# Optimization experiments

Hardware: AMD Instinct MI355X
Metric: run time of the kernel (lower is better)

The kernel has to match this reference:

```python
import jax, jax.numpy as jnp
import numpy as np

B, C, H, W = 4, 512, 32, 32
HEADS = 8
EPS = 1e-5


def setup_inputs() -> dict:
    key = jax.random.key(0)
    ks = jax.random.split(key, 9)
    s = 1.0 / np.sqrt(C)
    return {
        "x": jax.random.normal(ks[0], (B, C, H, W), dtype=jnp.float32),
        "w_q": jax.random.normal(ks[1], (C, C), dtype=jnp.float32) * s,  # Conv2d 1x1, no bias
        "w_k": jax.random.normal(ks[2], (C, C), dtype=jnp.float32) * s,
        "w_v": jax.random.normal(ks[3], (C, C), dtype=jnp.float32) * s,
        "w_head": jax.random.normal(ks[4], (HEADS, HEADS), dtype=jnp.float32) * (1.0 / np.sqrt(HEADS)),
        "in_gamma": jnp.ones((HEADS,), dtype=jnp.float32) + 0.1 * jax.random.normal(ks[5], (HEADS,), dtype=jnp.float32),
        "in_beta": 0.1 * jax.random.normal(ks[6], (HEADS,), dtype=jnp.float32),
        "w_proj": jax.random.normal(ks[7], (C, C), dtype=jnp.float32) * s,
        "b_proj": 0.02 * jax.random.normal(ks[8], (C,), dtype=jnp.float32),
    }


def reference(x, w_q, w_k, w_v, w_head, in_gamma, in_beta, w_proj, b_proj):
    b, c, h, w = x.shape
    heads = w_head.shape[0]
    hd = c // heads
    t = h * w
    scale = hd ** (-0.5)

    xf = x.reshape(b, c, t)  # [B,C,T]
    # 1x1 convs == channel matmuls
    q = jnp.einsum('oc,bct->bot', w_q, xf).reshape(b, heads, hd, t)
    k = jnp.einsum('oc,bct->bot', w_k, xf).reshape(b, heads, hd, t)
    v = jnp.einsum('oc,bct->bot', w_v, xf).reshape(b, heads, hd, t)

    attn = jnp.einsum('bhdq,bhdT->bhqT', q, k) * scale           # [B,heads,T,T]
    attn = jnp.einsum('gh,bhqT->bgqT', w_head, attn)             # head-mixing 1x1 conv
    attn = jax.nn.softmax(attn, axis=-1)
    # InstanceNorm2d over the (T,T) spatial dims, per head, biased variance
    mean = jnp.mean(attn, axis=(-2, -1), keepdims=True)
    var = jnp.var(attn, axis=(-2, -1), keepdims=True)
    attn = (attn - mean) / jnp.sqrt(var + EPS)
    attn = attn * in_gamma[None, :, None, None] + in_beta[None, :, None, None]

    out = jnp.einsum('bhqT,bhdT->bhqd', attn, v)                 # [B,heads,T,hd]
    out = out.reshape(b, t, c)                                   # same row-major flatten as torch .view
    out = out @ w_proj.T + b_proj                                # Linear
    return out.transpose(0, 2, 1).reshape(b, c, h, w)
```

## Files before the change

kernel.cpp:

```cpp
#include <hip/hip_runtime.h>
#include <hip/hip_bf16.h>

#define B_ 4
#define C_ 512
#define T_ 1024
#define SCALE_ 0.125f
#define EPS_ 1e-5f

typedef unsigned short u16;
typedef __attribute__((ext_vector_type(8))) unsigned short u16x8;
typedef __attribute__((ext_vector_type(4))) unsigned short u16x4;
typedef __attribute__((ext_vector_type(8))) short s16x8;
typedef __attribute__((ext_vector_type(4))) float f32x4;

#define QT_OFF    (0x0ull)
#define KS_OFF    (0x400000ull)
#define VS_OFF    (0x800000ull)
#define XT_OFF    (0xC00000ull)
#define O_OFF     (0x1000000ull)
#define AB_OFF    (0x1410000ull)
#define VSUM_OFF  (0x1420000ull)
#define BIAS2_OFF (0x1430000ull)
#define LSUM_OFF  (0x1440000ull)
#define L2SUM_OFF (0x1460000ull)
#define WB_OFF    (0x1480000ull)
#define LP_OFF    (0x1680000ull)
#define L2P_OFF   (0x1700000ull)
#define WS_OFF    (0x1780000ull)
#define OP_OFF    (0x2000000ull)

static __device__ __forceinline__ u16 f2bf(float f) {
  unsigned u = __float_as_uint(f);
  unsigned r = (u + 0x7fff + ((u >> 16) & 1)) >> 16;
  return (u16)r;
}
static __device__ __forceinline__ float b2f(u16 x) {
  return __uint_as_float(((unsigned)x) << 16);
}
static __device__ __forceinline__ f32x4 mfma16(s16x8 a, s16x8 b, f32x4 c) {
  return __builtin_amdgcn_mfma_f32_16x16x32_bf16(a, b, c, 0, 0, 0);
}

__global__ __launch_bounds__(256) void prep_k(
    const float* __restrict__ x, const float* __restrict__ wq,
    const float* __restrict__ wk, const float* __restrict__ wv,
    const float* __restrict__ wp, u16* __restrict__ wb,
    float* __restrict__ ws, float* __restrict__ vsum, u16* __restrict__ xt) {
  const int id = blockIdx.x;
  const int tid = threadIdx.x;
  __shared__ float Ts[64][65];
  if (id < 512) {
    const int i = (id << 8) + tid;
    const int idx = i << 3;
    const int which = idx >> 18;
    const int off = idx & 262143;
    const float* s = which == 0 ? wq : which == 1 ? wk : which == 2 ? wv : wp;
    const float4 f0 = *(const float4*)(s + off);
    const float4 f1 = *(const float4*)(s + off + 4);
    u16x8 o;
    o[0] = f2bf(f0.x); o[1] = f2bf(f0.y); o[2] = f2bf(f0.z); o[3] = f2bf(f0.w);
    o[4] = f2bf(f1.x); o[5] = f2bf(f1.y); o[6] = f2bf(f1.z); o[7] = f2bf(f1.w);
    *(u16x8*)(wb + idx) = o;
  } else if (id < 640) {
    const int idx = ((id - 512) << 8) + tid;
    if (id - 512 < 8) vsum[idx] = 0.f;
    const int o = idx >> 6, d = idx & 63;
    float s = 0.f;
#pragma unroll
    for (int j = 0; j < 8; ++j) s += wp[(o << 9) + (j << 6) + d];
    ws[idx] = s;
  } else {
    const int id3 = id - 640;
    const int b = id3 >> 7, rem = id3 & 127;
    const int t0 = (rem & 15) << 6;
    const int c0 = (rem >> 4) << 6;
    const float* __restrict__ X = x + (size_t)b * (C_ * (size_t)T_);
    u16* __restrict__ Xt = xt + (size_t)b * (T_ * (size_t)C_);
#pragma unroll
    for (int i = 0; i < 4; ++i) {
      const int e = tid + (i << 8);
      const int r = e >> 4, c4 = e & 15;
      const float4 v =
          *(const float4*)(X + (size_t)(c0 + r) * T_ + t0 + (c4 << 2));
      Ts[r][(c4 << 2) + 0] = v.x; Ts[r][(c4 << 2) + 1] = v.y;
      Ts[r][(c4 << 2) + 2] = v.z; Ts[r][(c4 << 2) + 3] = v.w;
    }
    __syncthreads();
#pragma unroll
    for (int i = 0; i < 2; ++i) {
      const int e = tid + (i << 8);
      const int tt = e >> 3, c8 = e & 7;
      u16x8 o;
#pragma unroll
      for (int j = 0; j < 8; ++j) o[j] = f2bf(Ts[(c8 << 3) + j][tt]);
      *(u16x8*)(Xt + (size_t)(t0 + tt) * C_ + c0 + (c8 << 3)) = o;
    }
  }
}

__global__ __launch_bounds__(256) void gemm_qkv(
    const u16* __restrict__ xt, const u16* __restrict__ wqb,
    const u16* __restrict__ wkb, const u16* __restrict__ wvb,
    u16* __restrict__ qto, u16* __restrict__ ks, u16* __restrict__ vs) {
  const int z = blockIdx.z;
  const int tid = threadIdx.x;
  const int w = tid >> 6, lane = tid & 63, lr = lane & 15, lq = lane >> 4;
  const int wm = (w >> 1) << 6, wn = (w & 1) << 6;
  __shared__ u16 As[128][72];
  __shared__ u16 Bs[128][72];
  const u16 *Ag, *Bg;
  int m0, n0, mode, b;
  if (z < 8) {
    const int which = z >> 2;
    b = z & 3;
    Ag = xt + (size_t)b * (T_ * (size_t)C_);
    m0 = blockIdx.x << 7;
    Bg = which ? wkb : wqb;
    n0 = blockIdx.y << 7;
    mode = which;
  } else {
    b = z - 8;
    Ag = wvb;
    m0 = blockIdx.y << 7;
    Bg = xt + (size_t)b * (T_ * (size_t)C_);
    n0 = blockIdx.x << 7;
    mode = 2;
  }
  f32x4 acc[4][4] = {};
  for (int k0 = 0; k0 < C_; k0 += 64) {
#pragma unroll
    for (int it = 0; it < 4; ++it) {
      const int e = tid + (it << 8);
      const int r = e >> 3, c8 = (e & 7) << 3;
      *(u16x8*)&As[r][c8] =
          *(const u16x8*)(Ag + (size_t)(m0 + r) * C_ + k0 + c8);
      *(u16x8*)&Bs[r][c8] =
          *(const u16x8*)(Bg + (size_t)(n0 + r) * C_ + k0 + c8);
    }
    __syncthreads();
#pragma unroll
    for (int kf = 0; kf < 2; ++kf) {
      const int ko = (kf << 5) + (lq << 3);
      s16x8 a[4], bb[4];
#pragma unroll
      for (int i = 0; i < 4; ++i) a[i] = *(const s16x8*)&As[wm + (i << 4) + lr][ko];
#pragma unroll
      for (int j = 0; j < 4; ++j) bb[j] = *(const s16x8*)&Bs[wn + (j << 4) + lr][ko];
#pragma unroll
      for (int i = 0; i < 4; ++i)
#pragma unroll
        for (int j = 0; j < 4; ++j) acc[i][j] = mfma16(a[i], bb[j], acc[i][j]);
    }
    __syncthreads();
  }
  if (mode == 0) {
    u16* Y = qto + (size_t)b * (T_ * (size_t)C_);
#pragma unroll
    for (int i = 0; i < 4; ++i) {
      const int row = wm + (i << 4) + (lq << 2);
#pragma unroll
      for (int j = 0; j < 4; ++j) {
        const int col = wn + (j << 4) + lr;
#pragma unroll
        for (int r = 0; r < 4; ++r)
          Y[(size_t)(m0 + row + r) * C_ + n0 + col] =
              f2bf(acc[i][j][r] * SCALE_);
      }
    }
  } else if (mode == 1) {
#pragma unroll
    for (int i = 0; i < 4; ++i) {
#pragma unroll
      for (int j = 0; j < 4; ++j) {
        const int o = n0 + wn + (j << 4) + lr;
        const int f = o >> 5, quadk = (o >> 3) & 3, e = o & 7;
#pragma unroll
        for (int r = 0; r < 4; ++r) {
          const int t = m0 + wm + (i << 4) + (lq << 2) + r;
          const int t32 = t >> 5, rr = t & 31;
          const int half = (rr >> 2) & 1;
          const int lrk = ((rr >> 3) << 2) | (rr & 3);
          const size_t idx =
              ((((size_t)((((b << 5) | t32) << 1) | half) << 4 | f) << 6 |
                (quadk << 4) | lrk)
               << 3) |
              e;
          ks[idx] = f2bf(acc[i][j][r]);
        }
      }
    }
  } else {
#pragma unroll
    for (int i = 0; i < 4; ++i) {
#pragma unroll
      for (int j = 0; j < 4; ++j) {
        const int t = n0 + wn + (j << 4) + lr;
        const int t32 = t >> 5, quadv = (t >> 3) & 3, e = t & 7;
#pragma unroll
        for (int r = 0; r < 4; ++r) {
          const int o = m0 + wm + (i << 4) + (lq << 2) + r;
          const int g = o >> 6, dj = (o >> 4) & 3, lrv = o & 15;
          const size_t idx =
              ((((size_t)((((b << 3) | g) << 5) | t32) << 2 | dj) << 6 |
                (quadv << 4) | lrv)
               << 3) |
              e;
          vs[idx] = f2bf(acc[i][j][r]);
        }
      }
    }
  }
}

__global__ __launch_bounds__(256) void vsum_k(const u16* __restrict__ vs,
                                              float* __restrict__ vsum) {
  const int bg = blockIdx.x;
  const int tcb = blockIdx.y;
  const int tid = threadIdx.x;
  const int d = tid >> 2, part = tid & 3;
  const int dj = d >> 4, lrv = d & 15;
  const int t32 = (tcb << 2) + part;
  const u16* __restrict__ p = vs + (((size_t)bg) << 16) + ((size_t)t32 << 11) +
                              (dj << 9) + (lrv << 3);
  float s = 0.f;
#pragma unroll
  for (int q = 0; q < 4; ++q) {
    const u16x8 x = *(const u16x8*)(p + (q << 7));
#pragma unroll
    for (int j = 0; j < 8; ++j) s += b2f(x[j]);
  }
  s += __shfl_down(s, 2, 64);
  s += __shfl_down(s, 1, 64);
  if (part == 0) atomicAdd(&vsum[(bg << 6) + d], s);
}

__global__ __launch_bounds__(512, 4) void attn_fused(
    const u16* __restrict__ Qt, const u16* __restrict__ KS,
    const u16* __restrict__ VS, const float* __restrict__ wh,
    float* __restrict__ Opart, float* __restrict__ lpart,
    float* __restrict__ l2part) {
  const int id = blockIdx.x;
  const int xcd = id & 7;
  const int b = xcd >> 1;
  const int hi = id >> 3;
  const int qb = ((xcd & 1) << 5) | (hi & 31);
  const int tq = hi >> 5;
  const int q0 = qb << 4;
  const int tid = threadIdx.x;
  const int w = tid >> 6, lane = tid & 63;
  const int lr = lane & 15, quad = lane >> 4;

  __shared__ __align__(16) u16 Qs[16][522];
  __shared__ __align__(16) u16 Plds[8][16][136];
  float* Sbuf = (float*)&Plds[0][0][0];

  {
    const u16* Qb = Qt + ((size_t)b * T_ + q0) * C_;
    for (int i = tid; i < 1024; i += 512) {
      const int r = i >> 6, c8 = i & 63;
      *(u16x8*)&Qs[r][c8 << 3] = *(const u16x8*)(Qb + (size_t)r * C_ + (c8 << 3));
    }
  }

  const u16* __restrict__ Qrow = &Qs[lr][quad << 3];
  const int g = w;
  const int win = w >> 1, half = w & 1;
  const u16* __restrict__ Vc =
      VS + (((size_t)((b << 3) | g)) << 16) + (lane << 3);

  float lacc[8] = {}, l2acc[8] = {};
  f32x4 acc[4] = {};

  __syncthreads();

  for (int c = 0; c < 2; ++c) {
    const int t32k = (tq << 3) + (c << 2) + win;
    const u16* __restrict__ Kc =
        KS + (((size_t)((((b << 5) | t32k) << 1) | half)) << 13) + (lane << 3);
    f32x4 m[8] = {};
#pragma unroll 2
    for (int h = 0; h < 8; ++h) {
      f32x4 a0 = {0.f, 0.f, 0.f, 0.f};
      const s16x8 qf0 = *(const s16x8*)(Qrow + (h << 6));
      const s16x8 k0 = *(const s16x8*)(Kc + (h << 10));
      a0 = mfma16(k0, qf0, a0);
      const s16x8 qf1 = *(const s16x8*)(Qrow + (h << 6) + 32);
      const s16x8 k1 = *(const s16x8*)(Kc + (h << 10) + 512);
      a0 = mfma16(k1, qf1, a0);
#pragma unroll
      for (int gg = 0; gg < 8; ++gg) {
        const float wgh = wh[(gg << 3) + h];
        m[gg] += a0 * wgh;
      }
    }
#pragma unroll
    for (int gg = 0; gg < 8; ++gg) {
      f32x4 e0;
#pragma unroll
      for (int k = 0; k < 4; ++k) e0[k] = __expf(m[gg][k]);
      u16x4 o;
#pragma unroll
      for (int k = 0; k < 4; ++k) o[k] = f2bf(e0[k]);
      *(u16x4*)&Plds[gg][lr][(win << 5) + (quad << 3) + (half << 2)] = o;
      lacc[gg] += e0[0] + e0[1] + e0[2] + e0[3];
      l2acc[gg] += e0[0] * e0[0] + e0[1] * e0[1] + e0[2] * e0[2] + e0[3] * e0[3];
    }
    __syncthreads();
#pragma unroll
    for (int tw = 0; tw < 4; ++tw) {
      const int t32v = (tq << 3) + (c << 2) + tw;
      const s16x8 pa = *(const s16x8*)&Plds[g][lr][(tw << 5) + (quad << 3)];
#pragma unroll
      for (int dj = 0; dj < 4; ++dj) {
        const s16x8 vb =
            *(const s16x8*)(Vc + ((size_t)t32v << 11) + (dj << 9));
        acc[dj] = mfma16(pa, vb, acc[dj]);
      }
    }
    __syncthreads();
  }

  const int bg = (b << 3) + g;
  const size_t obase = ((((size_t)(tq << 5) + bg) << 10) + q0) * 64;
#pragma unroll
  for (int dj = 0; dj < 4; ++dj) {
    const int d = (dj << 4) + lr;
#pragma unroll
    for (int r = 0; r < 4; ++r) {
      const int q = (quad << 2) + r;
      Opart[obase + (size_t)q * 64 + d] = acc[dj][r];
    }
  }

  float* lbuf = Sbuf;
  float* l2buf = Sbuf + 1024;
#pragma unroll
  for (int gg = 0; gg < 8; ++gg) {
    float l = lacc[gg];
    l += __shfl_xor(l, 16, 64);
    l += __shfl_xor(l, 32, 64);
    float l2 = l2acc[gg];
    l2 += __shfl_xor(l2, 16, 64);
    l2 += __shfl_xor(l2, 32, 64);
    if (quad == 0) {
      lbuf[(w << 7) + (gg << 4) + lr] = l;
      l2buf[(w << 7) + (gg << 4) + lr] = l2;
    }
  }
  __syncthreads();
  if (lane < 16) {
    float l = 0.f, l2 = 0.f;
#pragma unroll
    for (int w2 = 0; w2 < 8; ++w2) {
      l += lbuf[(w2 << 7) + (g << 4) + lr];
      l2 += l2buf[(w2 << 7) + (g << 4) + lr];
    }
    const size_t li = (((size_t)(tq << 5) + bg) << 10) + q0 + lr;
    lpart[li] = l;
    l2part[li] = l2;
  }
}

__global__ __launch_bounds__(256) void combine_o(
    const float* __restrict__ Opart, const float* __restrict__ lpart,
    const float* __restrict__ l2part, u16* __restrict__ O,
    float* __restrict__ lsum, float* __restrict__ l2sum) {
  const int bg = blockIdx.x;
  const int qo = blockIdx.y;
  const int tid = threadIdx.x;
  const int q = (qo << 7) + (tid >> 1);
  const int d0 = (tid & 1) << 5;
  float l = 0.f, l2 = 0.f;
#pragma unroll
  for (int tq = 0; tq < 4; ++tq) {
    const size_t li = (((size_t)(tq << 5) + bg) << 10) + q;
    l += lpart[li];
    l2 += l2part[li];
  }
  const float linv = 1.f / l;
  if ((tid & 1) == 0) {
    lsum[((size_t)bg << 10) + q] = l;
    l2sum[((size_t)bg << 10) + q] = l2;
  }
  f32x4 a[8] = {};
#pragma unroll
  for (int tq = 0; tq < 4; ++tq) {
    const float* src =
        Opart + ((((size_t)(tq << 5) + bg) << 10) + q) * 64 + d0;
#pragma unroll
    for (int j = 0; j < 8; ++j) a[j] += *(const f32x4*)(src + (j << 2));
  }
  u16* dst = O + (((size_t)bg << 10) + q) * 64 + d0;
#pragma unroll
  for (int j = 0; j < 4; ++j) {
    u16x8 o;
#pragma unroll
    for (int k = 0; k < 4; ++k) {
      o[k] = f2bf(a[2 * j][k] * linv);
      o[k + 4] = f2bf(a[2 * j + 1][k] * linv);
    }
    *(u16x8*)(dst + (j << 3)) = o;
  }
}

__global__ __launch_bounds__(256) void stats_k(const float* __restrict__ lsum,
                                               const float* __restrict__ l2sum,
                                               const float* __restrict__ gamma,
                                               const float* __restrict__ beta,
                                               const float* __restrict__ ws,
                                               const float* __restrict__ bp,
                                               const float* __restrict__ vsum,
                                               float* __restrict__ ab,
                                               float* __restrict__ bias2) {
  const int bg = blockIdx.x;
  const int g = bg & 7;
  const int tid = threadIdx.x;
  const f32x4 l = *(const f32x4*)(lsum + ((size_t)bg << 10) + (tid << 2));
  const f32x4 l2 = *(const f32x4*)(l2sum + ((size_t)bg << 10) + (tid << 2));
  float ssq = 0.f;
#pragma unroll
  for (int k = 0; k < 4; ++k) ssq += l2[k] / (l[k] * l[k]);
#pragma unroll
  for (int off = 32; off; off >>= 1) ssq += __shfl_xor(ssq, off, 64);
  __shared__ float red[4];
  __shared__ float bt2s;
  if ((tid & 63) == 0) red[tid >> 6] = ssq;
  __syncthreads();
  if (tid == 0) {
    const float s = red[0] + red[1] + red[2] + red[3];
    const float mean = 0.0009765625f;
    const float var = s * (1.f / 1048576.f) - mean * mean;
    const float al = gamma[g] * rsqrtf(var + EPS_);
    const float bt2 = beta[g] - al * mean;
    ab[bg * 2] = al;
    ab[bg * 2 + 1] = bt2;
    bt2s = bt2;
  }
  __syncthreads();
  const float bt2 = bt2s;
  const float* vs = vsum + (bg << 6);
#pragma unroll
  for (int oo = 0; oo < 2; ++oo) {
    const int o = tid + (oo << 8);
    const float* wr = ws + (o << 6);
    float acc = 0.f;
#pragma unroll
    for (int d = 0; d < 64; d += 4) {
      const float4 vv4 = *(const float4*)(vs + d);
      const float4 ws4 = *(const float4*)(wr + d);
      acc += ws4.x * vv4.x + ws4.y * vv4.y + ws4.z * vv4.z + ws4.w * vv4.w;
    }
    bias2[(bg << 9) + o] = bp[o] + bt2 * acc;
  }
}

__global__ __launch_bounds__(256) void gemm_proj(const u16* __restrict__ O,
                                                 const u16* __restrict__ wpb,
                                                 const float* __restrict__ ab,
                                                 const float* __restrict__ bias2,
                                                 float* __restrict__ y) {
  const int b = blockIdx.z;
  const int m0 = blockIdx.y << 7;
  const int n0 = blockIdx.x << 7;
  const int g = blockIdx.x;
  const u16* __restrict__ Ob = O + (size_t)b * (8 * T_ * 64);
  __shared__ u16 As[128][72];
  __shared__ u16 Bs[128][72];
  const int tid = threadIdx.x;
  const int w = tid >> 6, lane = tid & 63, lr = lane & 15, lq = lane >> 4;
  const int wm = (w >> 1) << 6, wn = (w & 1) << 6;
  f32x4 acc[4][4] = {};
  for (int k0 = 0; k0 < C_; k0 += 64) {
#pragma unroll
    for (int it = 0; it < 4; ++it) {
      const int e = tid + (it << 8);
      const int r = e >> 3, c8 = (e & 7) << 3;
      *(u16x8*)&As[r][c8] =
          *(const u16x8*)(wpb + (size_t)(m0 + r) * C_ + k0 + c8);
      const int t = n0 + r;
      const int c = k0 + c8;
      *(u16x8*)&Bs[r][c8] =
          *(const u16x8*)(Ob + (size_t)(t >> 7) * (T_ * 64) +
                          (size_t)(((t & 127) << 3) + (c >> 6)) * 64 + (c & 63));
    }
    __syncthreads();
#pragma unroll
    for (int kf = 0; kf < 2; ++kf) {
      const int ko = (kf << 5) + (lq << 3);
      s16x8 a[4], bb[4];
#pragma unroll
      for (int i = 0; i < 4; ++i) a[i] = *(const s16x8*)&As[wm + (i << 4) + lr][ko];
#pragma unroll
      for (int j = 0; j < 4; ++j) bb[j] = *(const s16x8*)&Bs[wn + (j << 4) + lr][ko];
#pragma unroll
      for (int i = 0; i < 4; ++i)
#pragma unroll
        for (int j = 0; j < 4; ++j) acc[i][j] = mfma16(a[i], bb[j], acc[i][j]);
    }
    __syncthreads();
  }
  const float al = ab[(((b << 3) + g) << 1)];
  const float* __restrict__ b2 = bias2 + (((b << 3) + g) << 9);
#pragma unroll
  for (int i = 0; i < 4; ++i) {
    const int row = wm + (i << 4) + (lq << 2);
#pragma unroll
    for (int j = 0; j < 4; ++j) {
      const int col = wn + (j << 4) + lr;
#pragma unroll
      for (int r = 0; r < 4; ++r)
        y[(size_t)b * (C_ * (size_t)T_) + (size_t)(m0 + row + r) * T_ + n0 + col] =
            acc[i][j][r] * al + b2[m0 + row + r];
    }
  }
}

extern "C" void kernel_launch(void* const* d_in, const int* in_sizes, int n_in,
                              void* d_out, int out_size, void* d_ws,
                              size_t ws_size, hipStream_t stream) {
  const float* x = (const float*)d_in[0];
  const float* wq = (const float*)d_in[1];
  const float* wk = (const float*)d_in[2];
  const float* wv = (const float*)d_in[3];
  const float* wh = (const float*)d_in[4];
  const float* gm = (const float*)d_in[5];
  const float* bt = (const float*)d_in[6];
  const float* wp = (const float*)d_in[7];
  const float* bp = (const float*)d_in[8];
  float* y = (float*)d_out;
  char* wsb = (char*)d_ws;

  u16* Qt = (u16*)(wsb + QT_OFF);
  u16* KS = (u16*)(wsb + KS_OFF);
  u16* VS = (u16*)(wsb + VS_OFF);
  u16* Xt = (u16*)(wsb + XT_OFF);
  u16* Og = (u16*)(wsb + O_OFF);
  float* ab = (float*)(wsb + AB_OFF);
  float* vsum = (float*)(wsb + VSUM_OFF);
  float* bias2 = (float*)(wsb + BIAS2_OFF);
  float* lsum = (float*)(wsb + LSUM_OFF);
  float* l2sum = (float*)(wsb + L2SUM_OFF);
  u16* Wb = (u16*)(wsb + WB_OFF);
  u16* WQb = Wb;
  u16* WKb = Wb + 262144;
  u16* WVb = Wb + 524288;
  u16* WPb = Wb + 786432;
  float* lpart = (float*)(wsb + LP_OFF);
  float* l2part = (float*)(wsb + L2P_OFF);
  float* ws = (float*)(wsb + WS_OFF);
  float* Opart = (float*)(wsb + OP_OFF);

  prep_k<<<dim3(1152), 256, 0, stream>>>(x, wq, wk, wv, wp, Wb, ws, vsum, Xt);
  gemm_qkv<<<dim3(8, 4, 12), 256, 0, stream>>>(Xt, WQb, WKb, WVb, Qt, KS, VS);
  vsum_k<<<dim3(32, 8), 256, 0, stream>>>(VS, vsum);
  attn_fused<<<dim3(1024), 512, 0, stream>>>(Qt, KS, VS, wh, Opart, lpart,
                                             l2part);
  combine_o<<<dim3(32, 8), 256, 0, stream>>>(Opart, lpart, l2part, Og, lsum,
                                             l2sum);
  stats_k<<<dim3(32), 256, 0, stream>>>(lsum, l2sum, gm, bt, ws, bp, vsum, ab,
                                        bias2);
  gemm_proj<<<dim3(8, 4, 4), 256, 0, stream>>>(Og, WPb, ab, bias2, y);
}
```

Before: 169.9 us.

## Fuse V row-sum into QKV GEMM and stage K/V swizzled stores through LDS

The separate vsum kernel is removed. The V-projection epilogue now reduces its accumulators across lanes and adds the per-channel sums into vsum with atomics. The K and V epilogues, which used to write scattered 2-byte elements into the swizzled layouts, now write the tile to shared memory first and emit 16-byte vector stores. This saves a kernel launch and a full reread of V, and makes the global writes coalesced, at the cost of extra LDS traffic and a barrier. The attention score loop's unroll factor is also raised from 2 to 4.

```diff
diff --git a/kernel.cpp b/kernel.cpp
--- a/kernel.cpp
+++ b/kernel.cpp
@@ -101,13 +101,14 @@
 __global__ __launch_bounds__(256) void gemm_qkv(
     const u16* __restrict__ xt, const u16* __restrict__ wqb,
     const u16* __restrict__ wkb, const u16* __restrict__ wvb,
-    u16* __restrict__ qto, u16* __restrict__ ks, u16* __restrict__ vs) {
+    u16* __restrict__ qto, u16* __restrict__ ks, u16* __restrict__ vs,
+    float* __restrict__ vsum) {
   const int z = blockIdx.z;
   const int tid = threadIdx.x;
   const int w = tid >> 6, lane = tid & 63, lr = lane & 15, lq = lane >> 4;
   const int wm = (w >> 1) << 6, wn = (w & 1) << 6;
-  __shared__ u16 As[128][72];
-  __shared__ u16 Bs[128][72];
+  __shared__ __align__(16) u16 S[2][128][72];
+  u16* Ts = &S[0][0][0];
   const u16 *Ag, *Bg;
   int m0, n0, mode, b;
   if (z < 8) {
@@ -132,9 +133,9 @@
     for (int it = 0; it < 4; ++it) {
       const int e = tid + (it << 8);
       const int r = e >> 3, c8 = (e & 7) << 3;
-      *(u16x8*)&As[r][c8] =
+      *(u16x8*)&S[0][r][c8] =
           *(const u16x8*)(Ag + (size_t)(m0 + r) * C_ + k0 + c8);
-      *(u16x8*)&Bs[r][c8] =
+      *(u16x8*)&S[1][r][c8] =
           *(const u16x8*)(Bg + (size_t)(n0 + r) * C_ + k0 + c8);
     }
     __syncthreads();
@@ -143,9 +144,9 @@
       const int ko = (kf << 5) + (lq << 3);
       s16x8 a[4], bb[4];
 #pragma unroll
-      for (int i = 0; i < 4; ++i) a[i] = *(const s16x8*)&As[wm + (i << 4) + lr][ko];
-#pragma unroll
-      for (int j = 0; j < 4; ++j) bb[j] = *(const s16x8*)&Bs[wn + (j << 4) + lr][ko];
+      for (int i = 0; i < 4; ++i) a[i] = *(const s16x8*)&S[0][wm + (i << 4) + lr][ko];
+#pragma unroll
+      for (int j = 0; j < 4; ++j) bb[j] = *(const s16x8*)&S[1][wn + (j << 4) + lr][ko];
 #pragma unroll
       for (int i = 0; i < 4; ++i)
 #pragma unroll
@@ -167,71 +168,63 @@
               f2bf(acc[i][j][r] * SCALE_);
       }
     }
-  } else if (mode == 1) {
-#pragma unroll
-    for (int i = 0; i < 4; ++i) {
-#pragma unroll
-      for (int j = 0; j < 4; ++j) {
-        const int o = n0 + wn + (j << 4) + lr;
-        const int f = o >> 5, quadk = (o >> 3) & 3, e = o & 7;
-#pragma unroll
-        for (int r = 0; r < 4; ++r) {
-          const int t = m0 + wm + (i << 4) + (lq << 2) + r;
-          const int t32 = t >> 5, rr = t & 31;
-          const int half = (rr >> 2) & 1;
-          const int lrk = ((rr >> 3) << 2) | (rr & 3);
-          const size_t idx =
-              ((((size_t)((((b << 5) | t32) << 1) | half) << 4 | f) << 6 |
-                (quadk << 4) | lrk)
-               << 3) |
-              e;
-          ks[idx] = f2bf(acc[i][j][r]);
+    return;
+  }
+  if (mode == 2) {
+#pragma unroll
+    for (int i = 0; i < 4; ++i)
+#pragma unroll
+      for (int r = 0; r < 4; ++r) {
+        float s = acc[i][0][r] + acc[i][1][r] + acc[i][2][r] + acc[i][3][r];
+        s += __shfl_xor(s, 1, 64);
+        s += __shfl_xor(s, 2, 64);
+        s += __shfl_xor(s, 4, 64);
+        s += __shfl_xor(s, 8, 64);
+        if (lr == 0) {
+          const int o = m0 + wm + (i << 4) + (lq << 2) + r;
+          atomicAdd(&vsum[(((b << 3) | (o >> 6)) << 6) | (o & 63)], s);
         }
       }
+  }
+#pragma unroll
+  for (int i = 0; i < 4; ++i)
+#pragma unroll
+    for (int j = 0; j < 4; ++j)
+#pragma unroll
+      for (int r = 0; r < 4; ++r)
+        Ts[(wm + (i << 4) + (lq << 2) + r) * 136 + wn + (j << 4) + lr] =
+            f2bf(acc[i][j][r]);
+  __syncthreads();
+  if (mode == 1) {
+    const int t32l = tid >> 6, half = (tid >> 5) & 1, fl = (tid >> 3) & 3,
+              part = tid & 7;
+    const int t32g = (m0 >> 5) + t32l, fg = (n0 >> 5) + fl;
+    u16* dst =
+        ks + (((((size_t)((b << 5) | t32g) << 1) | half) << 4 | fg) << 9);
+#pragma unroll
+    for (int u = 0; u < 8; ++u) {
+      const int lanek = (u << 3) + part;
+      const int quadk = lanek >> 4, lrk = lanek & 15;
+      const int rr = ((lrk >> 2) << 3) | (half << 2) | (lrk & 3);
+      const u16x8 v = *(const u16x8*)&Ts[((t32l << 5) + rr) * 136 + (fl << 5) +
+                                         (quadk << 3)];
+      *(u16x8*)(dst + (lanek << 3)) = v;
     }
   } else {
-#pragma unroll
-    for (int i = 0; i < 4; ++i) {
-#pragma unroll
-      for (int j = 0; j < 4; ++j) {
-        const int t = n0 + wn + (j << 4) + lr;
-        const int t32 = t >> 5, quadv = (t >> 3) & 3, e = t & 7;
-#pragma unroll
-        for (int r = 0; r < 4; ++r) {
-          const int o = m0 + wm + (i << 4) + (lq << 2) + r;
-          const int g = o >> 6, dj = (o >> 4) & 3, lrv = o & 15;
-          const size_t idx =
-              ((((size_t)((((b << 3) | g) << 5) | t32) << 2 | dj) << 6 |
-                (quadv << 4) | lrv)
-               << 3) |
-              e;
-          vs[idx] = f2bf(acc[i][j][r]);
-        }
-      }
-    }
-  }
-}
-
-__global__ __launch_bounds__(256) void vsum_k(const u16* __restrict__ vs,
-                                              float* __restrict__ vsum) {
-  const int bg = blockIdx.x;
-  const int tcb = blockIdx.y;
-  const int tid = threadIdx.x;
-  const int d = tid >> 2, part = tid & 3;
-  const int dj = d >> 4, lrv = d & 15;
-  const int t32 = (tcb << 2) + part;
-  const u16* __restrict__ p = vs + (((size_t)bg) << 16) + ((size_t)t32 << 11) +
-                              (dj << 9) + (lrv << 3);
-  float s = 0.f;
-#pragma unroll
-  for (int q = 0; q < 4; ++q) {
-    const u16x8 x = *(const u16x8*)(p + (q << 7));
-#pragma unroll
-    for (int j = 0; j < 8; ++j) s += b2f(x[j]);
-  }
-  s += __shfl_down(s, 2, 64);
-  s += __shfl_down(s, 1, 64);
-  if (part == 0) atomicAdd(&vsum[(bg << 6) + d], s);
+    const int gl = tid >> 7, t32l = (tid >> 5) & 3, dj = (tid >> 3) & 3,
+              part = tid & 7;
+    const int gg = (m0 >> 6) + gl, t32g = (n0 >> 5) + t32l;
+    u16* dst =
+        vs + (((((size_t)((b << 3) | gg) << 5) | t32g) << 2 | dj) << 9);
+#pragma unroll
+    for (int u = 0; u < 8; ++u) {
+      const int lanev = (u << 3) + part;
+      const int quadv = lanev >> 4, lrv = lanev & 15;
+      const u16x8 v = *(const u16x8*)&Ts[((gl << 6) + (dj << 4) + lrv) * 136 +
+                                         (t32l << 5) + (quadv << 3)];
+      *(u16x8*)(dst + (lanev << 3)) = v;
+    }
+  }
 }
 
 __global__ __launch_bounds__(512, 4) void attn_fused(
@@ -278,7 +271,7 @@
     const u16* __restrict__ Kc =
         KS + (((size_t)((((b << 5) | t32k) << 1) | half)) << 13) + (lane << 3);
     f32x4 m[8] = {};
-#pragma unroll 2
+#pragma unroll 4
     for (int h = 0; h < 8; ++h) {
       f32x4 a0 = {0.f, 0.f, 0.f, 0.f};
       const s16x8 qf0 = *(const s16x8*)(Qrow + (h << 6));
@@ -551,8 +544,8 @@
   float* Opart = (float*)(wsb + OP_OFF);
 
   prep_k<<<dim3(1152), 256, 0, stream>>>(x, wq, wk, wv, wp, Wb, ws, vsum, Xt);
-  gemm_qkv<<<dim3(8, 4, 12), 256, 0, stream>>>(Xt, WQb, WKb, WVb, Qt, KS, VS);
-  vsum_k<<<dim3(32, 8), 256, 0, stream>>>(VS, vsum);
+  gemm_qkv<<<dim3(8, 4, 12), 256, 0, stream>>>(Xt, WQb, WKb, WVb, Qt, KS, VS,
+                                               vsum);
   attn_fused<<<dim3(1024), 512, 0, stream>>>(Qt, KS, VS, wh, Opart, lpart,
                                              l2part);
   combine_o<<<dim3(32, 8), 256, 0, stream>>>(Opart, lpart, l2part, Og, lsum,
```

New measurement: 169.3 us. About the same (-0.4%).
